# Optimization experiments

Measured on AMD Instinct MI355X. Metric: run time of the kernel, lower is better.

Reference implementation:

```python
import jax, jax.numpy as jnp
import numpy as np

# ---- constants derived from init kwargs ----
XB = (-30.0, 30.0, 0.15); YB = (-15.0, 15.0, 0.15)
NX = np.array([(XB[1]-XB[0])/XB[2], (YB[1]-YB[0])/YB[2]], np.float32)   # [400, 200]
DX = np.array([XB[2], YB[2]], np.float32)
BX = np.array([XB[0]+XB[2]/2.0, YB[0]+YB[2]/2.0], np.float32)
BOUND = DX/2.0 - BX                                                      # [30, 15]
CDIST_THR = float(np.linalg.norm(1.5/(2.0*BOUND)))
NUM_CLASSES = 3
B, N, G, PTS_PER_INS = 16, 1024, 1024, 32


def setup_inputs() -> dict:
    key = jax.random.key(0)
    k1, k2, k3, k4, k5 = jax.random.split(key, 5)
    # matches/semantics are log-probs (NLLLoss expects log-space inputs)
    matches = jax.nn.log_softmax(jax.random.normal(k1, (B, N+1, N+1), jnp.float32), axis=-1)
    positions = jax.random.uniform(k2, (B, N, 2), jnp.float32) * (jnp.asarray(NX) - 1.0)
    semantics = jax.nn.log_softmax(jax.random.normal(k3, (B, NUM_CLASSES, N), jnp.float32), axis=1)
    masks = jnp.ones((B, N, 1), jnp.float32)
    # raw GT points in metric coords in [-bound, bound]
    gt_pts = (jax.random.uniform(k4, (B, G, 2), jnp.float32) * 2.0 - 1.0) * jnp.asarray(BOUND)
    gt_ins = jnp.broadcast_to(jnp.arange(G, dtype=jnp.int32) // PTS_PER_INS, (B, G))
    gt_order = jnp.broadcast_to(jnp.arange(G, dtype=jnp.int32) % PTS_PER_INS, (B, G))
    gt_type = jax.random.randint(k5, (B, G), 0, NUM_CLASSES, dtype=jnp.int32)
    return {"matches": matches, "positions": positions, "semantics": semantics,
            "masks": masks, "gt_pts": gt_pts, "gt_ins": gt_ins,
            "gt_order": gt_order, "gt_type": gt_type}


def _per_sample(match, position, semantic, gt_pts, gt_ins, gt_order, gt_type):
    nx = jnp.asarray(NX, position.dtype)
    bound = jnp.asarray(BOUND, position.dtype)
    n = position.shape[0]
    pos = position / (nx - 1.0)                        # [N,2] normalized preds
    pgt = (gt_pts + bound) / (2.0 * bound)             # [G,2] normalized GT
    # cdist pred->gt, nearest GT per prediction
    cd = jnp.sqrt(jnp.sum((pos[:, None, :] - pgt[None, :, :])**2, -1) + 1e-12)  # [N,G]
    nearest = jnp.argmin(cd, 1)                        # [N]
    ndist = jnp.min(cd, 1)
    ins = jnp.where(ndist < CDIST_THR, gt_ins[nearest], -1)   # instance id or -1
    order = gt_order[nearest]
    # group preds by instance, sort by within-instance order (stable by index),
    # connect consecutive members: match_gt[prev, next] = 1
    perm = jnp.lexsort((jnp.arange(n), order, ins))    # primary key = ins
    a, b = perm[:-1], perm[1:]
    same = (ins[a] == ins[b]) & (ins[a] >= 0)
    M = jnp.zeros((n + 1, n + 1), match.dtype)
    M = M.at[a, b].add(same.astype(match.dtype))       # (a,b) pairs are unique
    # conflict resolution: each column keeps only the closest (in pred space) row
    dist_map = jnp.sqrt(jnp.sum((pos[:, None, :] - pos[None, :, :])**2, -1) + 1e-12)  # [N,N]
    blk = M[:n, :n]
    colsum = blk.sum(0)
    best = jnp.argmin(jnp.where(blk > 0, dist_map, jnp.inf), 0)             # [N]
    newblk = jax.nn.one_hot(best, n, dtype=match.dtype).T * (colsum > 0)    # [N,N]
    M = M.at[:n, :n].set(newblk)
    # dustbin assignments for unmatched rows/cols
    rowsum = M[:n, :].sum(1)
    M = M.at[:n, n].set((rowsum == 0).astype(match.dtype))
    colsum2 = M[:, :n].sum(0)
    M = M.at[n, :n].set((colsum2 == 0).astype(match.dtype))
    # NLL match losses (forward/backward direction), dustbin row/col excluded from targets
    t_back = jnp.argmax(M, 0)[:n]                      # per column: matched row
    t_fwd = jnp.argmax(M, 1)[:n]                       # per row: matched col
    j = jnp.arange(n)
    mloss = -jnp.mean(match[j, t_fwd]) - jnp.mean(match[j, t_back])
    # semantic gt from nearest GT type (no distance threshold, as in original)
    sem_cls = gt_type[nearest]                         # [N]
    sg = jax.nn.one_hot(sem_cls, NUM_CLASSES, dtype=semantic.dtype).T   # [C,N]
    semloss = -jnp.mean(semantic[sem_cls, j])
    closs = jnp.mean(jnp.abs(pos - pgt[nearest]))
    return closs, mloss, semloss, M, sg


def reference(matches, positions, semantics, masks, gt_pts, gt_ins, gt_order, gt_type):
    # masks assumed all-ones (full validity), so boolean compaction is identity
    closs, mloss, semloss, matches_gt, semantics_gt = jax.vmap(_per_sample)(
        matches, positions, semantics, gt_pts, gt_ins, gt_order, gt_type)
    return (jnp.mean(closs), jnp.mean(mloss), jnp.mean(semloss), matches_gt, semantics_gt)
```

## Files before the change

kernel.cpp:

```cpp
#include <hip/hip_runtime.h>
#include <math.h>

#define BB 16
#define NN 1024
#define GG 1024
#define NP1 1025
#define NC 3

__device__ __forceinline__ void get_consts(float& bnd0, float& bnd1,
                                           float& tb0, float& tb1, float& thr) {
    const float bx0 = (float)(-30.0 + 0.15 / 2.0);
    const float bx1 = (float)(-15.0 + 0.15 / 2.0);
    bnd0 = __fsub_rn(__fmul_rn(0.15f, 0.5f), bx0);
    bnd1 = __fsub_rn(__fmul_rn(0.15f, 0.5f), bx1);
    tb0 = __fmul_rn(2.0f, bnd0); tb1 = __fmul_rn(2.0f, bnd1);
    const float q0 = __fdiv_rn(1.5f, tb0), q1 = __fdiv_rn(1.5f, tb1);
    thr = __fsqrt_rn(__fadd_rn(__fmul_rn(q0, q0), __fmul_rn(q1, q1)));
}

__global__ __launch_bounds__(512) void k_near(
    const float* __restrict__ positions, const float* __restrict__ gt_pts,
    const int* __restrict__ gt_ins, const int* __restrict__ gt_order,
    const int* __restrict__ gt_type,
    int* __restrict__ key_ws, int* __restrict__ sem_ws,
    int* __restrict__ tf_ws, int* __restrict__ tb_ws,
    float* __restrict__ closs_part)
{
    __shared__ float2 sp[GG];
    __shared__ unsigned long long pl[512];
    const int b = blockIdx.y, pc = blockIdx.x, tid = threadIdx.x;
    const int sub = tid & 63, gs = tid >> 6;
    float bnd0, bnd1, tb0, tb1, thr;
    get_consts(bnd0, bnd1, tb0, tb1, thr);

    for (int g = tid; g < GG; g += 512) {
        float2 gp = ((const float2*)gt_pts)[b * GG + g];
        float2 pg;
        pg.x = __fdiv_rn(__fadd_rn(gp.x, bnd0), tb0);
        pg.y = __fdiv_rn(__fadd_rn(gp.y, bnd1), tb1);
        sp[g] = pg;
    }
    __syncthreads();

    const int i = (pc << 6) + sub;
    float2 p = ((const float2*)positions)[b * NN + i];
    const float px = __fdiv_rn(p.x, 399.0f);
    const float py = __fdiv_rn(p.y, 199.0f);

    unsigned long long best = ~0ull;
    const int gbase = gs << 7;
    #pragma unroll 8
    for (int j = 0; j < 128; ++j) {
        float2 pg = sp[gbase + j];
        float dx = __fsub_rn(px, pg.x);
        float dy = __fsub_rn(py, pg.y);
        float s  = __fadd_rn(__fadd_rn(__fmul_rn(dx, dx), __fmul_rn(dy, dy)), 1e-12f);
        float cd = __fsqrt_rn(s);
        unsigned long long pk =
            ((unsigned long long)__float_as_uint(cd) << 10) | (unsigned)(gbase + j);
        best = (pk < best) ? pk : best;
    }
    pl[tid] = best;
    __syncthreads();
    #pragma unroll
    for (int s = 4; s > 0; s >>= 1) {
        if (gs < s) {
            unsigned long long v = pl[tid + (s << 6)];
            if (v < pl[tid]) pl[tid] = v;
        }
        __syncthreads();
    }

    if (tid < 64) {
        best = pl[tid];
        const int bi = (int)(best & 1023u);
        const float cd = __uint_as_float((unsigned)(best >> 10));

        const int ins = (cd < thr) ? gt_ins[b * GG + bi] : -1;
        const int key = ((ins + 1) << 15) | (gt_order[b * GG + bi] << 10) | i;
        key_ws[(b << 10) + i] = key;
        sem_ws[(b << 10) + i] = gt_type[b * GG + bi];
        tf_ws[(b << 10) + i] = NN;
        tb_ws[(b << 10) + i] = NN;

        float2 pg = sp[bi];
        float cl = fabsf(__fsub_rn(px, pg.x)) + fabsf(__fsub_rn(py, pg.y));
        #pragma unroll
        for (int s = 32; s > 0; s >>= 1) cl += __shfl_down(cl, s);
        if (tid == 0) closs_part[(b << 4) + pc] = cl;
    }
}

__global__ __launch_bounds__(128) void k_rank(
    const int* __restrict__ key_ws, int* __restrict__ sorted_ws)
{
    __shared__ int sk[NN];
    const int b = blockIdx.y, pc = blockIdx.x, tid = threadIdx.x;
    for (int j = tid; j < NN; j += 128) sk[j] = key_ws[(b << 10) + j];
    __syncthreads();
    const int k = sk[(pc << 7) + tid];
    int rank = 0;
    const int4* sk4 = (const int4*)sk;
    #pragma unroll 8
    for (int j = 0; j < 256; ++j) {
        int4 v = sk4[j];
        rank += (v.x < k) + (v.y < k) + (v.z < k) + (v.w < k);
    }
    sorted_ws[(b << 10) + rank] = k;
}

__global__ __launch_bounds__(512) void k_edges(
    const int* __restrict__ sorted_ws,
    int* __restrict__ tf_ws, int* __restrict__ tb_ws)
{
    const int b = blockIdx.y;
    const int p = (blockIdx.x << 9) + threadIdx.x;
    if (p >= NN - 1) return;
    const int k0 = sorted_ws[(b << 10) + p];
    const int k1 = sorted_ws[(b << 10) + p + 1];
    const int ia = (k0 >> 15) - 1;
    const int ic = (k1 >> 15) - 1;
    if (ia == ic && ia >= 0) {
        const int a = k0 & 1023, c = k1 & 1023;
        tf_ws[(b << 10) + a] = c;
        tb_ws[(b << 10) + c] = a;
    }
}

__global__ __launch_bounds__(256) void k_out(
    const float* __restrict__ matches, const float* __restrict__ semantics,
    const int* __restrict__ sem_ws,
    const int* __restrict__ tf_ws, const int* __restrict__ tb_ws,
    float* __restrict__ out, double* __restrict__ mpart, double* __restrict__ spart)
{
    const int b = blockIdx.y, pc = blockIdx.x, tid = threadIdx.x;
    float* Mb = out + 3 + (size_t)b * NP1 * NP1;

    {
        float* base = Mb + (size_t)pc * 32 * NP1;
        const int total = 32 * NP1;
        const int mis = (int)(((size_t)base >> 2) & 3);
        const int head = (4 - mis) & 3;
        const int n4 = (total - head) >> 2;
        const int tail = total - head - (n4 << 2);
        if (tid < head) base[tid] = 0.f;
        float4* b4 = (float4*)(base + head);
        float4 z; z.x = 0.f; z.y = 0.f; z.z = 0.f; z.w = 0.f;
        for (int k = tid; k < n4; k += 256) b4[k] = z;
        if (tid < tail) base[head + (n4 << 2) + tid] = 0.f;
    }
    __syncthreads();

    if (tid < 64) {
        double mv = 0.0, sv = 0.0;
        if (tid < 32) {
            const int i = (pc << 5) + tid;
            const int jf = tf_ws[(b << 10) + i];
            const int jb = tb_ws[(b << 10) + i];

            Mb[(size_t)i * NP1 + jf] = 1.0f;
            Mb[(size_t)NN * NP1 + i] = (jb == NN) ? 1.0f : 0.0f;
            if (pc == 0 && tid == 0) Mb[(size_t)NN * NP1 + NN] = 0.f;

            const float* mrow = matches + (size_t)b * NP1 * NP1 + (size_t)i * NP1;
            mv = (double)mrow[jf] + (double)mrow[jb];

            const int sc = sem_ws[(b << 10) + i];
            sv = (double)semantics[(b * NC + sc) * NN + i];

            float* sg = out + 3 + (size_t)BB * NP1 * NP1 + (size_t)b * NC * NN;
            sg[0 * NN + i] = (sc == 0) ? 1.0f : 0.0f;
            sg[1 * NN + i] = (sc == 1) ? 1.0f : 0.0f;
            sg[2 * NN + i] = (sc == 2) ? 1.0f : 0.0f;
        }
        #pragma unroll
        for (int s = 32; s > 0; s >>= 1) {
            mv += __shfl_down(mv, s);
            sv += __shfl_down(sv, s);
        }
        if (tid == 0) {
            mpart[(b << 5) + pc] = mv;
            spart[(b << 5) + pc] = sv;
        }
    }
}

__global__ __launch_bounds__(512) void k_final(
    const float* __restrict__ closs_part, const double* __restrict__ mpart,
    const double* __restrict__ spart, float* __restrict__ out)
{
    __shared__ double rc[512], rm[512], rs[512];
    const int t = threadIdx.x;
    rc[t] = (t < 256) ? (double)closs_part[t] : 0.0;
    rm[t] = mpart[t]; rs[t] = spart[t];
    __syncthreads();
    for (int s = 256; s > 0; s >>= 1) {
        if (t < s) { rc[t] += rc[t + s]; rm[t] += rm[t + s]; rs[t] += rs[t + s]; }
        __syncthreads();
    }
    if (t == 0) {
        out[0] = (float)(rc[0] / 32768.0);
        out[1] = (float)(-rm[0] / 16384.0);
        out[2] = (float)(-rs[0] / 16384.0);
    }
}

extern "C" void kernel_launch(void* const* d_in, const int* in_sizes, int n_in,
                              void* d_out, int out_size, void* d_ws, size_t ws_size,
                              hipStream_t stream) {
    const float* matches   = (const float*)d_in[0];
    const float* positions = (const float*)d_in[1];
    const float* semantics = (const float*)d_in[2];
    const float* gt_pts    = (const float*)d_in[4];
    const int*   gt_ins    = (const int*)d_in[5];
    const int*   gt_order  = (const int*)d_in[6];
    const int*   gt_type   = (const int*)d_in[7];
    float* out = (float*)d_out;

    char* ws = (char*)d_ws;
    int*    key_ws     = (int*)(ws + 0 * 65536);
    int*    sem_ws     = (int*)(ws + 1 * 65536);
    int*    sorted_ws  = (int*)(ws + 2 * 65536);
    int*    tf_ws      = (int*)(ws + 3 * 65536);
    int*    tb_ws      = (int*)(ws + 4 * 65536);
    float*  closs_part = (float*)(ws + 5 * 65536);
    double* mpart      = (double*)(ws + 5 * 65536 + 4096);
    double* spart      = (double*)(ws + 5 * 65536 + 8192);

    hipLaunchKernelGGL(k_near,  dim3(16, 16), dim3(512), 0, stream,
                       positions, gt_pts, gt_ins, gt_order, gt_type,
                       key_ws, sem_ws, tf_ws, tb_ws, closs_part);
    hipLaunchKernelGGL(k_rank,  dim3(8, 16),  dim3(128), 0, stream, key_ws, sorted_ws);
    hipLaunchKernelGGL(k_edges, dim3(2, 16),  dim3(512), 0, stream, sorted_ws, tf_ws, tb_ws);
    hipLaunchKernelGGL(k_out,   dim3(32, 16), dim3(256), 0, stream,
                       matches, semantics, sem_ws, tf_ws, tb_ws, out, mpart, spart);
    hipLaunchKernelGGL(k_final, dim3(1),      dim3(512), 0, stream,
                       closs_part, mpart, spart, out);
}
```

Baseline: 148.9 us.

## Replace rank-sort plus edge pass with direct successor search; fold final reduction

The rank-then-scatter sort and the separate edge-linking kernel are replaced by one kernel where each key finds its immediate successor with a min-reduction over all keys and writes the forward/backward links directly. The final reduction kernel is removed: closs is reduced inside the link kernel, and the match and semantic loss partials are accumulated into the output with float atomics. This cuts the launch count from five to three and drops a global sorted buffer. In exchange, the float atomics make summation order nondeterministic and accumulate in fp32 rather than double.

```diff
diff --git a/kernel.cpp b/kernel.cpp
--- a/kernel.cpp
+++ b/kernel.cpp
@@ -23,8 +23,7 @@
     const int* __restrict__ gt_ins, const int* __restrict__ gt_order,
     const int* __restrict__ gt_type,
     int* __restrict__ key_ws, int* __restrict__ sem_ws,
-    int* __restrict__ tf_ws, int* __restrict__ tb_ws,
-    float* __restrict__ closs_part)
+    int* __restrict__ tb_ws, float* __restrict__ closs_part)
 {
     __shared__ float2 sp[GG];
     __shared__ unsigned long long pl[512];
@@ -80,7 +79,6 @@
         const int key = ((ins + 1) << 15) | (gt_order[b * GG + bi] << 10) | i;
         key_ws[(b << 10) + i] = key;
         sem_ws[(b << 10) + i] = gt_type[b * GG + bi];
-        tf_ws[(b << 10) + i] = NN;
         tb_ws[(b << 10) + i] = NN;
 
         float2 pg = sp[bi];
@@ -91,39 +89,46 @@
     }
 }
 
-__global__ __launch_bounds__(128) void k_rank(
-    const int* __restrict__ key_ws, int* __restrict__ sorted_ws)
+__global__ __launch_bounds__(128) void k_link(
+    const int* __restrict__ key_ws,
+    int* __restrict__ tf_ws, int* __restrict__ tb_ws,
+    const float* __restrict__ closs_part, float* __restrict__ out)
 {
     __shared__ int sk[NN];
+    __shared__ float rcl[128];
     const int b = blockIdx.y, pc = blockIdx.x, tid = threadIdx.x;
     for (int j = tid; j < NN; j += 128) sk[j] = key_ws[(b << 10) + j];
     __syncthreads();
+
     const int k = sk[(pc << 7) + tid];
-    int rank = 0;
+    int succ = 0x7fffffff;
     const int4* sk4 = (const int4*)sk;
     #pragma unroll 8
     for (int j = 0; j < 256; ++j) {
         int4 v = sk4[j];
-        rank += (v.x < k) + (v.y < k) + (v.z < k) + (v.w < k);
-    }
-    sorted_ws[(b << 10) + rank] = k;
-}
-
-__global__ __launch_bounds__(512) void k_edges(
-    const int* __restrict__ sorted_ws,
-    int* __restrict__ tf_ws, int* __restrict__ tb_ws)
-{
-    const int b = blockIdx.y;
-    const int p = (blockIdx.x << 9) + threadIdx.x;
-    if (p >= NN - 1) return;
-    const int k0 = sorted_ws[(b << 10) + p];
-    const int k1 = sorted_ws[(b << 10) + p + 1];
-    const int ia = (k0 >> 15) - 1;
-    const int ic = (k1 >> 15) - 1;
-    if (ia == ic && ia >= 0) {
-        const int a = k0 & 1023, c = k1 & 1023;
-        tf_ws[(b << 10) + a] = c;
-        tb_ws[(b << 10) + c] = a;
+        succ = min(succ, (v.x > k) ? v.x : 0x7fffffff);
+        succ = min(succ, (v.y > k) ? v.y : 0x7fffffff);
+        succ = min(succ, (v.z > k) ? v.z : 0x7fffffff);
+        succ = min(succ, (v.w > k) ? v.w : 0x7fffffff);
+    }
+    const int i = k & 1023;
+    const bool edge = (succ != 0x7fffffff) &&
+                      ((succ >> 15) == (k >> 15)) && ((k >> 15) >= 1);
+    tf_ws[(b << 10) + i] = edge ? (succ & 1023) : NN;
+    if (edge) tb_ws[(b << 10) + (succ & 1023)] = i;
+
+    if (b == 0 && pc == 0) {
+        rcl[tid] = closs_part[tid] + closs_part[tid + 128];
+        __syncthreads();
+        for (int s = 64; s > 0; s >>= 1) {
+            if (tid < s) rcl[tid] += rcl[tid + s];
+            __syncthreads();
+        }
+        if (tid == 0) {
+            out[0] = (float)((double)rcl[0] / 32768.0);
+            out[1] = 0.f;
+            out[2] = 0.f;
+        }
     }
 }
 
@@ -131,7 +136,7 @@
     const float* __restrict__ matches, const float* __restrict__ semantics,
     const int* __restrict__ sem_ws,
     const int* __restrict__ tf_ws, const int* __restrict__ tb_ws,
-    float* __restrict__ out, double* __restrict__ mpart, double* __restrict__ spart)
+    float* __restrict__ out)
 {
     const int b = blockIdx.y, pc = blockIdx.x, tid = threadIdx.x;
     float* Mb = out + 3 + (size_t)b * NP1 * NP1;
@@ -179,29 +184,9 @@
             sv += __shfl_down(sv, s);
         }
         if (tid == 0) {
-            mpart[(b << 5) + pc] = mv;
-            spart[(b << 5) + pc] = sv;
-        }
-    }
-}
-
-__global__ __launch_bounds__(512) void k_final(
-    const float* __restrict__ closs_part, const double* __restrict__ mpart,
-    const double* __restrict__ spart, float* __restrict__ out)
-{
-    __shared__ double rc[512], rm[512], rs[512];
-    const int t = threadIdx.x;
-    rc[t] = (t < 256) ? (double)closs_part[t] : 0.0;
-    rm[t] = mpart[t]; rs[t] = spart[t];
-    __syncthreads();
-    for (int s = 256; s > 0; s >>= 1) {
-        if (t < s) { rc[t] += rc[t + s]; rm[t] += rm[t + s]; rs[t] += rs[t + s]; }
-        __syncthreads();
-    }
-    if (t == 0) {
-        out[0] = (float)(rc[0] / 32768.0);
-        out[1] = (float)(-rm[0] / 16384.0);
-        out[2] = (float)(-rs[0] / 16384.0);
+            atomicAdd(out + 1, (float)(-mv / 16384.0));
+            atomicAdd(out + 2, (float)(-sv / 16384.0));
+        }
     }
 }
 
@@ -220,20 +205,15 @@
     char* ws = (char*)d_ws;
     int*    key_ws     = (int*)(ws + 0 * 65536);
     int*    sem_ws     = (int*)(ws + 1 * 65536);
-    int*    sorted_ws  = (int*)(ws + 2 * 65536);
-    int*    tf_ws      = (int*)(ws + 3 * 65536);
-    int*    tb_ws      = (int*)(ws + 4 * 65536);
-    float*  closs_part = (float*)(ws + 5 * 65536);
-    double* mpart      = (double*)(ws + 5 * 65536 + 4096);
-    double* spart      = (double*)(ws + 5 * 65536 + 8192);
-
-    hipLaunchKernelGGL(k_near,  dim3(16, 16), dim3(512), 0, stream,
+    int*    tf_ws      = (int*)(ws + 2 * 65536);
+    int*    tb_ws      = (int*)(ws + 3 * 65536);
+    float*  closs_part = (float*)(ws + 4 * 65536);
+
+    hipLaunchKernelGGL(k_near, dim3(16, 16), dim3(512), 0, stream,
                        positions, gt_pts, gt_ins, gt_order, gt_type,
-                       key_ws, sem_ws, tf_ws, tb_ws, closs_part);
-    hipLaunchKernelGGL(k_rank,  dim3(8, 16),  dim3(128), 0, stream, key_ws, sorted_ws);
-    hipLaunchKernelGGL(k_edges, dim3(2, 16),  dim3(512), 0, stream, sorted_ws, tf_ws, tb_ws);
-    hipLaunchKernelGGL(k_out,   dim3(32, 16), dim3(256), 0, stream,
-                       matches, semantics, sem_ws, tf_ws, tb_ws, out, mpart, spart);
-    hipLaunchKernelGGL(k_final, dim3(1),      dim3(512), 0, stream,
-                       closs_part, mpart, spart, out);
-}
+                       key_ws, sem_ws, tb_ws, closs_part);
+    hipLaunchKernelGGL(k_link, dim3(8, 16),  dim3(128), 0, stream,
+                       key_ws, tf_ws, tb_ws, closs_part, out);
+    hipLaunchKernelGGL(k_out,  dim3(32, 16), dim3(256), 0, stream,
+                       matches, semantics, sem_ws, tf_ws, tb_ws, out);
+}
```

Result: slower. 158.3 us (+6.3%).
